# Kernel optimization log

Hardware: AMD Instinct MI355X
Metric: run time of the kernel (lower is better)

## Reference

```python
import jax, jax.numpy as jnp
import numpy as np

B, D, N, H = 2, 512, 2048, 8
DK = D // H
EPS = 1e-5


def conv1x1(x, w, b):
    # kernel-size-1 Conv1d == channel-mixing GEMM: (o,i) x (b,i,n) -> (b,o,n)
    return jnp.einsum('oi,bin->bon', w, x) + b[None, :, None]


def setup_inputs() -> dict:
    key = jax.random.key(0)
    ks = jax.random.split(key, 20)
    s = 0.02
    return {
        'init_query': jax.random.normal(ks[0], (B, D, N), jnp.float32),
        'key_t': jax.random.normal(ks[1], (B, D, N), jnp.float32),
        'value': jax.random.normal(ks[2], (B, D, N), jnp.float32),
        'mask': jax.random.randint(ks[3], (B, 1, N, N), 0, 2, jnp.int32),
        'Wq': jax.random.normal(ks[4], (D, D), jnp.float32) * s,
        'bq': jax.random.normal(ks[5], (D,), jnp.float32) * s,
        'Wk': jax.random.normal(ks[6], (D, D), jnp.float32) * s,
        'bk': jax.random.normal(ks[7], (D,), jnp.float32) * s,
        'Wv': jax.random.normal(ks[8], (D, D), jnp.float32) * s,
        'bv': jax.random.normal(ks[9], (D,), jnp.float32) * s,
        'Wm': jax.random.normal(ks[10], (D, D), jnp.float32) * s,
        'bm': jax.random.normal(ks[11], (D,), jnp.float32) * s,
        'W1': jax.random.normal(ks[12], (2 * D, 2 * D), jnp.float32) * s,
        'b1': jax.random.normal(ks[13], (2 * D,), jnp.float32) * s,
        'gamma': jnp.ones((2 * D,), jnp.float32),
        'beta': jnp.zeros((2 * D,), jnp.float32),
        'rmean': jax.random.normal(ks[14], (2 * D,), jnp.float32) * s,
        'rvar': jnp.abs(jax.random.normal(ks[15], (2 * D,), jnp.float32)) * 0.1 + 0.5,
        'W2': jax.random.normal(ks[16], (D, 2 * D), jnp.float32) * s,
        'b2': jnp.zeros((D,), jnp.float32),  # nn.init.constant_(bias, 0.0)
    }


def reference(init_query, key_t, value, mask, Wq, bq, Wk, bk, Wv, bv, Wm, bm,
              W1, b1, gamma, beta, rmean, rvar, W2, b2):
    # projections, split channels into (d_k, n_heads) exactly like torch .view
    q = conv1x1(init_query, Wq, bq).reshape(B, DK, H, N)
    k = conv1x1(key_t, Wk, bk).reshape(B, DK, H, N)
    v = conv1x1(value, Wv, bv).reshape(B, DK, H, N)
    scores = jnp.einsum('bdhn,bdhm->bhnm', q, k) / jnp.sqrt(jnp.float32(DK))
    scores = jnp.where(mask == 0, jnp.float32(-1e9), scores)
    attn = jax.nn.softmax(scores, axis=-1)
    x = jnp.einsum('bhnm,bdhm->bdhn', attn, v).reshape(B, D, N)
    x = conv1x1(x, Wm, bm)
    x = jnp.concatenate([x, init_query], axis=1)  # (B, 2D, N)
    h = conv1x1(x, W1, b1)
    # BatchNorm1d (inference mode with running stats) + ReLU
    h = (h - rmean[None, :, None]) * (gamma / jnp.sqrt(rvar + EPS))[None, :, None] + beta[None, :, None]
    h = jax.nn.relu(h)
    return conv1x1(h, W2, b2)
```

## Files before the change

### kernel.cpp

```cpp
#include <hip/hip_runtime.h>

typedef unsigned short u16;
typedef unsigned int u32;
typedef unsigned long long u64;
typedef long long i64;
typedef __bf16 bf16x8 __attribute__((ext_vector_type(8)));
typedef u16 u16x8 __attribute__((ext_vector_type(8)));
typedef float f32x4 __attribute__((ext_vector_type(4)));
typedef float f32x16 __attribute__((ext_vector_type(16)));

#define DEV __device__ __forceinline__

constexpr int BB = 2, DD = 512, NN = 2048, HH = 8, DKc = 64, D2 = 1024;

constexpr float QSC = 0.125f * 1.44269504088896340736f;

constexpr i64 MB = 1048576;
constexpr i64 OFF_CAT = 0;
constexpr i64 OFF_XKT = 8 * MB;
constexpr i64 OFF_XVT = 12 * MB;
constexpr i64 OFF_QH  = 16 * MB;
constexpr i64 OFF_KH  = 20 * MB;
constexpr i64 OFF_VT  = 24 * MB;
constexpr i64 OFF_HT  = 28 * MB;
constexpr i64 OFF_OP  = 36 * MB;
constexpr i64 OFF_LP  = 68 * MB;
constexpr i64 OFF_FLG = 68 * MB + 524288;
constexpr i64 OFF_WQP = 69 * MB;
constexpr i64 OFF_WKP = 69 * MB + 524288;
constexpr i64 OFF_WVP = 69 * MB + 1048576;
constexpr i64 OFF_WMT = 69 * MB + 1572864;
constexpr i64 OFF_W1A = 71 * MB;
constexpr i64 OFF_W1C = 72 * MB;
constexpr i64 OFF_W2B = 74 * MB;
constexpr i64 OFF_BQP = 75 * MB;
constexpr i64 OFF_BKP = 75 * MB + 2048;
constexpr i64 OFF_BVP = 75 * MB + 4096;
constexpr i64 OFF_BNA = 75 * MB + 8192;
constexpr i64 OFF_BNC = 75 * MB + 12288;
constexpr i64 OFF_MSK = 76 * MB;

DEV u16 f2bf(float f) {
  u32 u = __float_as_uint(f);
  u = u + 0x7FFFu + ((u >> 16) & 1u);
  return (u16)(u >> 16);
}

DEV float bf2f(u16 u) { return __uint_as_float(((u32)u) << 16); }
DEV float bf2f32(u32 u) { return __uint_as_float(u << 16); }

DEV u32 packbf(float lo, float hi) {
  return __builtin_amdgcn_perm(__float_as_uint(hi), __float_as_uint(lo), 0x07060302u);
}

DEV float fexp2(float x) {
#if __has_builtin(__builtin_amdgcn_exp2f)
  return __builtin_amdgcn_exp2f(x);
#else
  return exp2f(x);
#endif
}

DEV bf16x8 ldfrag(const u16* p) {
  bf16x8 v;
  __builtin_memcpy(&v, __builtin_assume_aligned(p, 16), 16);
  return v;
}

DEV bf16x8 ldfrag2(const u16* p0, const u16* p1) {
  bf16x8 v;
  __builtin_memcpy(&v, __builtin_assume_aligned(p0, 8), 8);
  __builtin_memcpy((char*)&v + 8, __builtin_assume_aligned(p1, 8), 8);
  return v;
}

DEV bf16x8 ones8() {
  u16x8 u = {0x3F80, 0x3F80, 0x3F80, 0x3F80, 0x3F80, 0x3F80, 0x3F80, 0x3F80};
  bf16x8 v;
  __builtin_memcpy(&v, &u, 16);
  return v;
}

DEV void gload16(const void* g, void* lds) {
  __builtin_amdgcn_global_load_lds((__attribute__((address_space(1))) void*)g,
                                   (__attribute__((address_space(3))) void*)lds, 16, 0, 0);
}

DEV f32x4 mfma16(bf16x8 a, bf16x8 b, f32x4 c) {
  return __builtin_amdgcn_mfma_f32_16x16x32_bf16(a, b, c, 0, 0, 0);
}

DEV f32x16 mfma32(bf16x8 a, bf16x8 b, f32x16 c) {
  return __builtin_amdgcn_mfma_f32_32x32x16_bf16(a, b, c, 0, 0, 0);
}

__global__ __launch_bounds__(256) void prep_all(
    const float* __restrict__ Wq, const float* __restrict__ Wk, const float* __restrict__ Wv,
    const float* __restrict__ Wm, const float* __restrict__ W1, const float* __restrict__ W2,
    const float* __restrict__ bq, const float* __restrict__ bk, const float* __restrict__ bv,
    const float* __restrict__ bm, const float* __restrict__ b1, const float* __restrict__ gamma_,
    const float* __restrict__ beta_, const float* __restrict__ rmean,
    const float* __restrict__ rvar, const int* __restrict__ mask,
    const float* __restrict__ iq, const float* __restrict__ kt, const float* __restrict__ vv,
    u16* __restrict__ wqp, u16* __restrict__ wkp, u16* __restrict__ wvp, u16* __restrict__ wmt,
    u16* __restrict__ w1a, u16* __restrict__ w1c, u16* __restrict__ w2b,
    float* __restrict__ bqp, float* __restrict__ bkp, float* __restrict__ bvp,
    float* __restrict__ bna, float* __restrict__ bnc, u32* __restrict__ mw,
    u32* __restrict__ flg,
    u16* __restrict__ cat, u16* __restrict__ xkt, u16* __restrict__ xvt) {
  __shared__ float tile[32][33];
  const int blk = blockIdx.x, t = threadIdx.x;
  if (blk < 768) {
    const int which = blk >> 8, lb = blk & 255;
    const float* W = which == 0 ? Wq : (which == 1 ? Wk : Wv);
    u16* dst = which == 0 ? wqp : (which == 1 ? wkp : wvp);
    for (int e = lb * 256 + t; e < 262144; e += 65536) {
      int op = e >> 9, i = e & 511;
      int dk = op & 63, h = op >> 6;
      dst[e] = f2bf(W[(dk * 8 + h) * 512 + i]);
    }
  } else if (blk < 1024) {
    const int lb = blk - 768;
    for (int e = lb * 256 + t; e < 262144; e += 65536) {
      int cp = e >> 9, o = e & 511;
      int dk = cp & 63, h = cp >> 6;
      wmt[e] = f2bf(Wm[o * 512 + dk * 8 + h]);
    }
  } else if (blk < 1280) {
    const int lb = blk - 1024;
    for (int e = lb * 256 + t; e < 524288; e += 65536) {
      int row = e >> 9, o = e & 511;
      w1a[e] = f2bf(W1[(i64)row * 1024 + o]);
    }
  } else if (blk < 1536) {
    const int lb = blk - 1280;
    for (int e = lb * 256 + t; e < 524288; e += 65536) {
      int row = e >> 9, j = e & 511;
      w1c[(i64)row * 1024 + 512 + j] = f2bf(W1[(i64)row * 1024 + 512 + j]);
    }
  } else if (blk < 1792) {
    const int lb = blk - 1536;
    for (int e = lb * 256 + t; e < 524288; e += 65536) w2b[e] = f2bf(W2[e]);
  } else if (blk < 1808) {
    __shared__ float sm[4][64];
    const int base = (blk - 1792) * 64;
    const int el = t & 63, oq = t >> 6;
    const float* wrow = W1 + (i64)(base + el) * 1024 + oq * 128;
    const float* bmq = bm + oq * 128;
    float s = 0.f;
#pragma unroll 8
    for (int j = 0; j < 128; j += 4) {
      float4 x = *(const float4*)(wrow + j);
      float4 y = *(const float4*)(bmq + j);
      s += x.x * y.x + x.y * y.y + x.z * y.z + x.w * y.w;
    }
    sm[oq][el] = s;
    __syncthreads();
    if (t < 64) {
      int e = base + t;
      float a = gamma_[e] * rsqrtf(rvar[e] + 1e-5f);
      bna[e] = a;
      bnc[e] = (b1[e] - rmean[e]) * a + beta_[e] + a * (sm[0][t] + sm[1][t] + sm[2][t] + sm[3][t]);
    }
  } else if (blk == 1808) {
    for (int e = t; e < 512; e += 256) {
      int src = (e & 63) * 8 + (e >> 6);
      bqp[e] = bq[src]; bkp[e] = bk[src]; bvp[e] = bv[src];
    }
    if (t < 128) flg[t] = 0u;
  } else if (blk < 2833) {
    const int tid = (blk - 1809) * 256 + t;
    const i64 base = (i64)tid * 32;
    const int4* mp = (const int4*)(mask + base);
    u32 word = 0;
#pragma unroll
    for (int j = 0; j < 8; ++j) {
      int4 x = mp[j];
      u32 nib = (x.x != 0 ? 1u : 0u) | (x.y != 0 ? 2u : 0u) | (x.z != 0 ? 4u : 0u) |
                (x.w != 0 ? 8u : 0u);
      word |= nib << (j * 4);
    }
    mw[tid] = word;
  } else {
    const int idx = blk - 2833;
    const int bx = idx & 63, by = (idx >> 6) & 15, bz = idx >> 10;
    const int tensor = bz >> 1, b = bz & 1;
    const float* src = (tensor == 0 ? iq : (tensor == 1 ? kt : vv)) + (i64)b * DD * NN;
    u16* dst; i64 ldd; int coff;
    if (tensor == 0)      { dst = cat + (i64)b * NN * D2; ldd = D2; coff = DD; }
    else if (tensor == 1) { dst = xkt + (i64)b * NN * DD; ldd = DD; coff = 0; }
    else                  { dst = xvt + (i64)b * NN * DD; ldd = DD; coff = 0; }
    const int x0 = bx * 32, y0 = by * 32;
    const int col = t & 31, rg = t >> 5;
#pragma unroll
    for (int i = 0; i < 4; ++i) {
      int row = rg + i * 8;
      tile[row][col] = src[(i64)(y0 + row) * NN + x0 + col];
    }
    __syncthreads();
    const int dp = t & 15, rbase = t >> 4;
    u32* dst32 = (u32*)dst;
    const i64 ldw = ldd >> 1;
    const int cw = (coff + y0) >> 1;
#pragma unroll
    for (int i = 0; i < 2; ++i) {
      int rr = rbase + i * 16;
      dst32[(i64)(x0 + rr) * ldw + cw + dp] = packbf(tile[2 * dp][rr], tile[2 * dp + 1][rr]);
    }
  }
}

template <int AM, int AN>
DEV void gemm_core(const u16* __restrict__ A, i64 lda, const u16* __restrict__ Bp, i64 ldb,
                   int K, u16* As, u16* Bs, f32x4 (&acc)[AM][AN]) {
  constexpr int BM = AM * 32, BN = AN * 32;
  const int t = threadIdx.x, w = t >> 6, l = t & 63, quad = l >> 4, l15 = l & 15;
  const int wm = (w >> 1) * AM * 16, wn = (w & 1) * AN * 16;
  auto stage = [&](int kk, int buf) {
    u16* Ad = As + buf * (BM * 64);
    u16* Bd = Bs + buf * (BN * 64);
#pragma unroll
    for (int j = 0; j < BM / 32; ++j) {
      int ch = j * 256 + w * 64 + l, r = ch >> 3, c = ch & 7;
      gload16(A + (i64)r * lda + kk + ((c ^ (r & 7)) << 3), Ad + (j * 256 + w * 64) * 8);
    }
#pragma unroll
    for (int j = 0; j < BN / 32; ++j) {
      int ch = j * 256 + w * 64 + l, r = ch >> 3, c = ch & 7;
      gload16(Bp + (i64)r * ldb + kk + ((c ^ (r & 7)) << 3), Bd + (j * 256 + w * 64) * 8);
    }
  };
  const int nst = K >> 6;
  stage(0, 0);
  asm volatile("s_waitcnt vmcnt(0)" ::: "memory");
  __builtin_amdgcn_s_barrier();
  for (int s = 0; s < nst; ++s) {
    if (s + 1 < nst) stage((s + 1) << 6, (s + 1) & 1);
    const u16* Ac = As + (s & 1) * (BM * 64);
    const u16* Bc = Bs + (s & 1) * (BN * 64);
#pragma unroll
    for (int kc = 0; kc < 2; ++kc) {
      const int sw = ((kc * 4 + quad) ^ (l15 & 7)) << 3;
      bf16x8 af[AM], bfr[AN];
#pragma unroll
      for (int i = 0; i < AM; ++i) af[i] = ldfrag(&Ac[(wm + i * 16 + l15) * 64 + sw]);
#pragma unroll
      for (int j = 0; j < AN; ++j) bfr[j] = ldfrag(&Bc[(wn + j * 16 + l15) * 64 + sw]);
#pragma unroll
      for (int i = 0; i < AM; ++i)
#pragma unroll
        for (int j = 0; j < AN; ++j) acc[i][j] = mfma16(af[i], bfr[j], acc[i][j]);
    }
    asm volatile("s_waitcnt vmcnt(0) lgkmcnt(0)" ::: "memory");
    __builtin_amdgcn_s_barrier();
  }
}

__global__ __launch_bounds__(256) void qkv_gemm(const u16* __restrict__ cat,
                                                const u16* __restrict__ xkt,
                                                const u16* __restrict__ xvt,
                                                const u16* __restrict__ wqp,
                                                const u16* __restrict__ wkp,
                                                const u16* __restrict__ wvp,
                                                const u16* __restrict__ w1a,
                                                const u16* __restrict__ wmt,
                                                const float* __restrict__ bqp,
                                                const float* __restrict__ bkp,
                                                const float* __restrict__ bvp,
                                                u16* __restrict__ qh, u16* __restrict__ kh,
                                                u16* __restrict__ vt, u16* __restrict__ w1c) {
  __shared__ __align__(16) u16 As[2 * 128 * 64];
  __shared__ __align__(16) u16 Bs[2 * 128 * 64];
  const int flat = blockIdx.x;
  const int t = threadIdx.x, w = t >> 6, l = t & 63, quad = l >> 4, l15 = l & 15;
  const int wm = (w >> 1) * 64, wn = (w & 1) * 64;
  int op, b = 0, mx, ny;
  if (flat < 256) {
    op = flat >> 7;
    b = (flat >> 6) & 1;
    const int r = flat & 63;
    mx = r >> 2; ny = r & 3;
  } else if (flat < 384) {
    op = 2;
    const int r = flat - 256;
    b = r >> 6;
    const int rr = r & 63;
    mx = rr >> 4; ny = rr & 15;
  } else {
    op = 3;
    const int r = flat - 384;
    mx = r >> 2; ny = r & 3;
  }
  const u16 *A, *Bp;
  i64 lda, ldb;
  if (op < 2) {
    A = (op == 0 ? cat + DD : xkt);
    lda = (op == 0 ? D2 : DD);
    A += (i64)b * NN * lda + (i64)mx * 128 * lda;
    Bp = (op == 0 ? wqp : wkp) + (i64)ny * 128 * DD;
    ldb = DD;
  } else if (op == 2) {
    A = wvp + (i64)mx * 128 * DD; lda = DD;
    Bp = xvt + (i64)b * NN * DD + (i64)ny * 128 * DD; ldb = DD;
  } else {
    A = w1a + (i64)mx * 128 * DD; lda = DD;
    Bp = wmt + (i64)ny * 128 * DD; ldb = DD;
  }
  f32x4 acc[4][4] = {};
  gemm_core<4, 4>(A, lda, Bp, ldb, DD, As, Bs, acc);

  const int rowBase = mx * 128 + wm + quad * 4;
  const int colBase = ny * 128 + wn + l15;
  if (op < 2) {
    const float* bias = (op == 0 ? bqp : bkp);
    const float sc = (op == 0 ? QSC : 1.f);
    u16* dst = (op == 0 ? qh : kh) + (i64)b * HH * NN * DKc;
#pragma unroll
    for (int j = 0; j < 4; ++j) {
      const int col = colBase + j * 16;
      const float cA = bias[col];
#pragma unroll
      for (int i = 0; i < 4; ++i)
#pragma unroll
        for (int r = 0; r < 4; ++r) {
          const int row = rowBase + i * 16 + r;
          dst[(i64)(col >> 6) * (NN * 64) + (i64)row * 64 + (col & 63)] =
              f2bf((acc[i][j][r] + cA) * sc);
        }
    }
  } else if (op == 2) {
    u16* dst = vt + (i64)b * HH * DKc * NN;
#pragma unroll
    for (int j = 0; j < 4; ++j) {
      const int col = colBase + j * 16;
#pragma unroll
      for (int i = 0; i < 4; ++i)
#pragma unroll
        for (int r = 0; r < 4; ++r) {
          const int row = rowBase + i * 16 + r;
          dst[(i64)row * NN + col] = f2bf(acc[i][j][r] + bvp[row]);
        }
    }
  } else {
#pragma unroll
    for (int j = 0; j < 4; ++j) {
      const int col = colBase + j * 16;
#pragma unroll
      for (int i = 0; i < 4; ++i)
#pragma unroll
        for (int r = 0; r < 4; ++r) {
          const int row = rowBase + i * 16 + r;
          w1c[(i64)row * D2 + col] = f2bf(acc[i][j][r]);
        }
    }
  }
}

struct GArgs {
  const u16* A; i64 lda, sAb;
  const u16* B; i64 ldb, sBb;
  void* C; i64 ldc, sCb;
  const float* p1; const float* p2;
  int K;
};

template <int MODE, int AM, int AN, int SWZ>
__global__ __launch_bounds__(256) void gemm_bt(GArgs g) {
  __shared__ __align__(16) u16 As[2 * AM * 32 * 64];
  __shared__ __align__(16) u16 Bs[2 * AN * 32 * 64];
  const int t = threadIdx.x, w = t >> 6, l = t & 63, quad = l >> 4, l15 = l & 15;
  const int wm = (w >> 1) * AM * 16, wn = (w & 1) * AN * 16;
  int bx = blockIdx.x, by = blockIdx.y, bz = blockIdx.z;
  if (SWZ == 1) {
    const int i = bx + (by << 3) + (bz << 8);
    const int slot = i & 7, jj = i >> 3;
    by = slot + ((jj & 3) << 3);
    const int j2 = jj >> 2;
    bx = j2 & 7;
    bz = j2 >> 3;
  }
  const u16* A = g.A + (i64)bz * g.sAb + (i64)bx * (AM * 32) * g.lda;
  const u16* Bp = g.B + (i64)bz * g.sBb + (i64)by * (AN * 32) * g.ldb;
  f32x4 acc[AM][AN] = {};
  gemm_core<AM, AN>(A, g.lda, Bp, g.ldb, g.K, As, Bs, acc);

  const int rowBase = bx * (AM * 32) + wm + quad * 4;
  const int colBase = by * (AN * 32) + wn + l15;
#pragma unroll
  for (int j = 0; j < AN; ++j) {
    const int col = colBase + j * 16;
    float cA = 0.f, cB = 0.f;
    if (MODE == 3) { cA = g.p1[col]; cB = g.p2[col]; }
#pragma unroll
    for (int i = 0; i < AM; ++i) {
#pragma unroll
      for (int r = 0; r < 4; ++r) {
        const int row = rowBase + i * 16 + r;
        float v = acc[i][j][r];
        if (MODE == 3) {
          float x = v * cA + cB;
          ((u16*)g.C + (i64)bz * g.sCb)[(i64)row * g.ldc + col] = f2bf(x > 0.f ? x : 0.f);
        } else {
          ((float*)g.C + (i64)bz * g.sCb)[(i64)row * g.ldc + col] = v + g.p1[row];
        }
      }
    }
  }
}

__global__ __launch_bounds__(512) void flash_attn(const u16* __restrict__ Qh,
                                                  const u16* __restrict__ Kh,
                                                  const u16* __restrict__ Vt,
                                                  const u64* __restrict__ MW64,
                                                  u16* __restrict__ Opart,
                                                  float* __restrict__ Lp,
                                                  u32* __restrict__ flags,
                                                  u16* __restrict__ cat) {
  __shared__ __align__(16) u16 smem[4 * 4096];
  u16* Ks0 = smem;
  u16* Ks1 = smem + 4096;
  u16* Vs0 = smem + 8192;
  u16* Vs1 = smem + 12288;
  const int t = threadIdx.x, w = t >> 6, l = t & 63, l31 = l & 31, lh = l >> 5;
  const int flat = blockIdx.x;
  const int h = flat & 7;
  const int j = flat >> 3;
  const int nt = j & 7, zz = j >> 3;
  const int sp = zz & 1, b = zz >> 1;
  const int nl = w * 32 + l31;
  const int n = nt * 256 + nl;
  const u16* Qb = Qh + ((i64)(b * HH + h) * NN + nt * 256 + w * 32) * 64;
  const u16* Kb = Kh + (i64)(b * HH + h) * NN * 64;
  const u16* Vb = Vt + (i64)(b * HH + h) * 64 * NN;
  const u64* mwp = MW64 + (i64)(b * NN + n) * 32;
  const bf16x8 ONE = ones8();
  bf16x8 qf[4];
#pragma unroll
  for (int kc = 0; kc < 4; ++kc)
    __builtin_memcpy(&qf[kc], Qb + (i64)l31 * 64 + kc * 16 + lh * 8, 16);

  f32x16 oacc0 = {}, oacc1 = {}, lacc = {};
  const int mt0 = sp * 16;

  auto stage = [&](u16* Kd, u16* Vd, int mt) {
    const int r = t >> 3, c = t & 7;
    gload16(Kb + (i64)(mt * 64 + r) * 64 + ((c ^ (r & 7)) << 3), Kd + t * 8);
    gload16(Vb + (i64)r * NN + mt * 64 + ((c ^ (r & 7)) << 3), Vd + t * 8);
  };
  auto compute = [&](const u16* Kc, const u16* Vc, int mt) {
    f32x16 s0 = {}, s1 = {};
    __builtin_amdgcn_s_setprio(1);
#pragma unroll
    for (int kc = 0; kc < 4; ++kc) {
      const int sw = l31 & 7;
      bf16x8 k0 = ldfrag(&Kc[l31 * 64 + (((kc * 2 + lh) ^ sw) << 3)]);
      bf16x8 k1 = ldfrag(&Kc[(32 + l31) * 64 + (((kc * 2 + lh) ^ sw) << 3)]);
      s0 = mfma32(k0, qf[kc], s0);
      s1 = mfma32(k1, qf[kc], s1);
    }
    __builtin_amdgcn_s_setprio(0);
    const u64 mrow = mwp[mt];
    u32 pw[16];
#pragma unroll
    for (int k = 0; k < 8; ++k) {
      const int kvb = ((2 * k) & 3) + 8 * ((2 * k) >> 2) + 4 * lh;
      u64 sh = mrow >> kvb;
      u32 mA = (((u32)sh & 1u) | (((u32)sh & 2u) << 15)) * 0xFFFFu;
      u32 shh = (u32)(sh >> 32);
      u32 mB = ((shh & 1u) | ((shh & 2u) << 15)) * 0xFFFFu;
      pw[k] = packbf(fexp2(s0[2 * k]), fexp2(s0[2 * k + 1])) & mA;
      pw[8 + k] = packbf(fexp2(s1[2 * k]), fexp2(s1[2 * k + 1])) & mB;
    }
    bf16x8 pf[4];
#pragma unroll
    for (int c = 0; c < 4; ++c) __builtin_memcpy(&pf[c], &pw[c * 4], 16);
    __builtin_amdgcn_s_setprio(1);
#pragma unroll
    for (int c = 0; c < 4; ++c) lacc = mfma32(ONE, pf[c], lacc);
#pragma unroll
    for (int c = 0; c < 4; ++c) {
      const int sw0 = l31 & 7;
      const u16* r0 = &Vc[l31 * 64];
      const u16* r1 = &Vc[(32 + l31) * 64];
      bf16x8 v0 = ldfrag2(r0 + (((2 * c) ^ sw0) << 3) + lh * 4,
                          r0 + (((2 * c + 1) ^ sw0) << 3) + lh * 4);
      bf16x8 v1 = ldfrag2(r1 + (((2 * c) ^ sw0) << 3) + lh * 4,
                          r1 + (((2 * c + 1) ^ sw0) << 3) + lh * 4);
      oacc0 = mfma32(v0, pf[c], oacc0);
      oacc1 = mfma32(v1, pf[c], oacc1);
    }
    __builtin_amdgcn_s_setprio(0);
  };

  stage(Ks0, Vs0, mt0);
  for (int ii = 0; ii < 8; ++ii) {
    const int m = mt0 + 2 * ii;
    __syncthreads();
    stage(Ks1, Vs1, m + 1);
    compute(Ks0, Vs0, m);
    __syncthreads();
    if (ii < 7) stage(Ks0, Vs0, m + 2);
    compute(Ks1, Vs1, m + 1);
  }

  u16* OpT = Opart + ((i64)((sp * BB + b) * HH + h) * 64) * NN;
#pragma unroll
  for (int r = 0; r < 16; ++r) {
    const int d0 = (r & 3) + 8 * (r >> 2) + 4 * lh;
    OpT[(i64)d0 * NN + n] = f2bf(oacc0[r]);
    OpT[(i64)(d0 + 32) * NN + n] = f2bf(oacc1[r]);
  }
  if (lh == 0) Lp[((i64)(sp * BB + b) * HH + h) * NN + n] = lacc[0];

  __shared__ u32 sflag;
  __syncthreads();
  if (t == 0) {
    __builtin_amdgcn_fence(__ATOMIC_RELEASE, "agent");
    const int pair = ((b * HH + h) << 3) | nt;
    sflag = atomicAdd(&flags[pair], 1u);
  }
  __syncthreads();
  if (sflag == 1u) {
    __builtin_amdgcn_fence(__ATOMIC_ACQUIRE, "agent");
    const int spo = sp ^ 1;
    const u16* OpP = Opart + ((i64)((spo * BB + b) * HH + h) * 64) * NN;
    const float lsum = lacc[0] + Lp[((i64)(spo * BB + b) * HH + h) * NN + n];
    const float rl = __builtin_amdgcn_rcpf(lsum);
    u32* lds32 = (u32*)smem;
#pragma unroll
    for (int e = 0; e < 8; ++e) {
      const int r0 = 2 * e, r1 = 2 * e + 1;
      const int d0 = (r0 & 3) + 8 * (r0 >> 2) + 4 * lh;
      const float a0 = oacc0[r0] + bf2f(OpP[(i64)d0 * NN + n]);
      const float a1 = oacc0[r1] + bf2f(OpP[(i64)(d0 + 1) * NN + n]);
      const float b0 = oacc1[r0] + bf2f(OpP[(i64)(d0 + 32) * NN + n]);
      const float b1 = oacc1[r1] + bf2f(OpP[(i64)(d0 + 33) * NN + n]);
      const int dp0 = d0 >> 1;
      lds32[nl * 32 + (dp0 ^ (nl & 31))] = packbf(a0 * rl, a1 * rl);
      lds32[nl * 32 + ((dp0 + 16) ^ (nl & 31))] = packbf(b0 * rl, b1 * rl);
    }
    __syncthreads();
    u32* catw = (u32*)cat;
#pragma unroll
    for (int i = 0; i < 16; ++i) {
      const int idx = i * 512 + t;
      const int nn = idx >> 5, dp = idx & 31;
      const u32 v = lds32[nn * 32 + (dp ^ (nn & 31))];
      catw[((i64)b * NN + nt * 256 + nn) * (D2 / 2) + h * 32 + dp] = v;
    }
  }
}

extern "C" void kernel_launch(void* const* d_in, const int* in_sizes, int n_in,
                              void* d_out, int out_size, void* d_ws, size_t ws_size,
                              hipStream_t stream) {
  (void)in_sizes; (void)n_in; (void)out_size; (void)ws_size;
  const float* iq    = (const float*)d_in[0];
  const float* kt    = (const float*)d_in[1];
  const float* vv    = (const float*)d_in[2];
  const int*   mask  = (const int*)d_in[3];
  const float* Wq    = (const float*)d_in[4];
  const float* bq    = (const float*)d_in[5];
  const float* Wk    = (const float*)d_in[6];
  const float* bk    = (const float*)d_in[7];
  const float* Wv    = (const float*)d_in[8];
  const float* bv    = (const float*)d_in[9];
  const float* Wm    = (const float*)d_in[10];
  const float* bm    = (const float*)d_in[11];
  const float* W1    = (const float*)d_in[12];
  const float* b1    = (const float*)d_in[13];
  const float* gamma_= (const float*)d_in[14];
  const float* beta_ = (const float*)d_in[15];
  const float* rmean = (const float*)d_in[16];
  const float* rvar  = (const float*)d_in[17];
  const float* W2    = (const float*)d_in[18];
  const float* b2    = (const float*)d_in[19];

  char* ws = (char*)d_ws;
  u16* cat = (u16*)(ws + OFF_CAT);
  u16* xkt = (u16*)(ws + OFF_XKT);
  u16* xvt = (u16*)(ws + OFF_XVT);
  u16* qh  = (u16*)(ws + OFF_QH);
  u16* kh  = (u16*)(ws + OFF_KH);
  u16* vt  = (u16*)(ws + OFF_VT);
  u16* ht  = (u16*)(ws + OFF_HT);
  u16* opart = (u16*)(ws + OFF_OP);
  float* lp  = (float*)(ws + OFF_LP);
  u32* flags = (u32*)(ws + OFF_FLG);
  u16* wqp = (u16*)(ws + OFF_WQP);
  u16* wkp = (u16*)(ws + OFF_WKP);
  u16* wvp = (u16*)(ws + OFF_WVP);
  u16* wmt = (u16*)(ws + OFF_WMT);
  u16* w1a = (u16*)(ws + OFF_W1A);
  u16* w1c = (u16*)(ws + OFF_W1C);
  u16* w2b = (u16*)(ws + OFF_W2B);
  float* bqp = (float*)(ws + OFF_BQP);
  float* bkp = (float*)(ws + OFF_BKP);
  float* bvp = (float*)(ws + OFF_BVP);
  float* bna = (float*)(ws + OFF_BNA);
  float* bnc = (float*)(ws + OFF_BNC);
  u32* mw = (u32*)(ws + OFF_MSK);

  prep_all<<<8977, 256, 0, stream>>>(Wq, Wk, Wv, Wm, W1, W2, bq, bk, bv, bm, b1, gamma_, beta_,
                                     rmean, rvar, mask, iq, kt, vv, wqp, wkp, wvp, wmt, w1a, w1c,
                                     w2b, bqp, bkp, bvp, bna, bnc, mw, flags, cat, xkt, xvt);
  qkv_gemm<<<416, 256, 0, stream>>>(cat, xkt, xvt, wqp, wkp, wvp, w1a, wmt,
                                    bqp, bkp, bvp, qh, kh, vt, w1c);
  flash_attn<<<256, 512, 0, stream>>>(qh, kh, vt, (const u64*)mw, opart, lp, flags, cat);
  GArgs wa{cat, D2, 0, w1c, D2, 0, ht, D2, 0, bna, bnc, D2};
  gemm_bt<3, 4, 2, 0><<<dim3(32, 16, 1), 256, 0, stream>>>(wa);
  GArgs w2a{w2b, D2, 0, ht, D2, (i64)NN * D2, d_out, NN, (i64)DD * NN, b2, nullptr, D2};
  gemm_bt<4, 2, 2, 1><<<dim3(8, 32, 2), 256, 0, stream>>>(w2a);
}
```

Measured before the change: 226.2 us.

## Split KV range within a block instead of across blocks with global merge

Previously each attention block handled 256 queries over half the keys and the two split blocks merged partial outputs through global memory, an atomic flag and fences. Now each block handles 128 queries over all keys, and its two wave halves each process alternate key sub-tiles, then merge partial sums through shared memory. This removes the global partial-output writes and reads, the atomic handshake and the flag initialisation. In exchange, shared memory use doubles to 64KB, each block runs twice as many KV iterations, and the in-block reduction adds barriers.

```diff
diff --git a/kernel.cpp b/kernel.cpp
--- a/kernel.cpp
+++ b/kernel.cpp
@@ -23,9 +23,6 @@
 constexpr i64 OFF_KH  = 20 * MB;
 constexpr i64 OFF_VT  = 24 * MB;
 constexpr i64 OFF_HT  = 28 * MB;
-constexpr i64 OFF_OP  = 36 * MB;
-constexpr i64 OFF_LP  = 68 * MB;
-constexpr i64 OFF_FLG = 68 * MB + 524288;
 constexpr i64 OFF_WQP = 69 * MB;
 constexpr i64 OFF_WKP = 69 * MB + 524288;
 constexpr i64 OFF_WVP = 69 * MB + 1048576;
@@ -106,7 +103,6 @@
     u16* __restrict__ w1a, u16* __restrict__ w1c, u16* __restrict__ w2b,
     float* __restrict__ bqp, float* __restrict__ bkp, float* __restrict__ bvp,
     float* __restrict__ bna, float* __restrict__ bnc, u32* __restrict__ mw,
-    u32* __restrict__ flg,
     u16* __restrict__ cat, u16* __restrict__ xkt, u16* __restrict__ xvt) {
   __shared__ float tile[32][33];
   const int blk = blockIdx.x, t = threadIdx.x;
@@ -167,7 +163,6 @@
       int src = (e & 63) * 8 + (e >> 6);
       bqp[e] = bq[src]; bkp[e] = bk[src]; bvp[e] = bv[src];
     }
-    if (t < 128) flg[t] = 0u;
   } else if (blk < 2833) {
     const int tid = (blk - 1809) * 256 + t;
     const i64 base = (i64)tid * 32;
@@ -412,24 +407,19 @@
                                                   const u16* __restrict__ Kh,
                                                   const u16* __restrict__ Vt,
                                                   const u64* __restrict__ MW64,
-                                                  u16* __restrict__ Opart,
-                                                  float* __restrict__ Lp,
-                                                  u32* __restrict__ flags,
                                                   u16* __restrict__ cat) {
-  __shared__ __align__(16) u16 smem[4 * 4096];
-  u16* Ks0 = smem;
-  u16* Ks1 = smem + 4096;
-  u16* Vs0 = smem + 8192;
-  u16* Vs1 = smem + 12288;
+  __shared__ __align__(16) u16 smem[4 * 8192];
+  u16* S0 = smem;
+  u16* S1 = smem + 16384;
   const int t = threadIdx.x, w = t >> 6, l = t & 63, l31 = l & 31, lh = l >> 5;
   const int flat = blockIdx.x;
   const int h = flat & 7;
   const int j = flat >> 3;
-  const int nt = j & 7, zz = j >> 3;
-  const int sp = zz & 1, b = zz >> 1;
-  const int nl = w * 32 + l31;
-  const int n = nt * 256 + nl;
-  const u16* Qb = Qh + ((i64)(b * HH + h) * NN + nt * 256 + w * 32) * 64;
+  const int nt = j & 15, b = j >> 4;
+  const int g = w & 3, half = w >> 2;
+  const int nl = g * 32 + l31;
+  const int n = nt * 128 + nl;
+  const u16* Qb = Qh + ((i64)(b * HH + h) * NN + nt * 128 + g * 32) * 64;
   const u16* Kb = Kh + (i64)(b * HH + h) * NN * 64;
   const u16* Vb = Vt + (i64)(b * HH + h) * 64 * NN;
   const u64* mwp = MW64 + (i64)(b * NN + n) * 32;
@@ -440,114 +430,107 @@
     __builtin_memcpy(&qf[kc], Qb + (i64)l31 * 64 + kc * 16 + lh * 8, 16);
 
   f32x16 oacc0 = {}, oacc1 = {}, lacc = {};
-  const int mt0 = sp * 16;
+  const int hrow = half * 32 + l31;
+  const int sw = l31 & 7;
 
   auto stage = [&](u16* Kd, u16* Vd, int mt) {
     const int r = t >> 3, c = t & 7;
     gload16(Kb + (i64)(mt * 64 + r) * 64 + ((c ^ (r & 7)) << 3), Kd + t * 8);
     gload16(Vb + (i64)r * NN + mt * 64 + ((c ^ (r & 7)) << 3), Vd + t * 8);
   };
-  auto compute = [&](const u16* Kc, const u16* Vc, int mt) {
-    f32x16 s0 = {}, s1 = {};
+  auto stage_pair = [&](u16* S, int mt) {
+    stage(S, S + 4096, mt);
+    stage(S + 8192, S + 12288, mt + 1);
+  };
+  auto compute_half = [&](const u16* Kc, const u16* Vc, int mt) {
+    f32x16 s = {};
     __builtin_amdgcn_s_setprio(1);
 #pragma unroll
     for (int kc = 0; kc < 4; ++kc) {
-      const int sw = l31 & 7;
-      bf16x8 k0 = ldfrag(&Kc[l31 * 64 + (((kc * 2 + lh) ^ sw) << 3)]);
-      bf16x8 k1 = ldfrag(&Kc[(32 + l31) * 64 + (((kc * 2 + lh) ^ sw) << 3)]);
-      s0 = mfma32(k0, qf[kc], s0);
-      s1 = mfma32(k1, qf[kc], s1);
+      bf16x8 k0 = ldfrag(&Kc[hrow * 64 + (((kc * 2 + lh) ^ sw) << 3)]);
+      s = mfma32(k0, qf[kc], s);
     }
     __builtin_amdgcn_s_setprio(0);
     const u64 mrow = mwp[mt];
-    u32 pw[16];
+    u32 pw[8];
 #pragma unroll
     for (int k = 0; k < 8; ++k) {
       const int kvb = ((2 * k) & 3) + 8 * ((2 * k) >> 2) + 4 * lh;
-      u64 sh = mrow >> kvb;
-      u32 mA = (((u32)sh & 1u) | (((u32)sh & 2u) << 15)) * 0xFFFFu;
-      u32 shh = (u32)(sh >> 32);
-      u32 mB = ((shh & 1u) | ((shh & 2u) << 15)) * 0xFFFFu;
-      pw[k] = packbf(fexp2(s0[2 * k]), fexp2(s0[2 * k + 1])) & mA;
-      pw[8 + k] = packbf(fexp2(s1[2 * k]), fexp2(s1[2 * k + 1])) & mB;
-    }
-    bf16x8 pf[4];
-#pragma unroll
-    for (int c = 0; c < 4; ++c) __builtin_memcpy(&pf[c], &pw[c * 4], 16);
+      const u32 m2 = (u32)(mrow >> (kvb + half * 32));
+      const u32 mA = ((m2 & 1u) | ((m2 & 2u) << 15)) * 0xFFFFu;
+      pw[k] = packbf(fexp2(s[2 * k]), fexp2(s[2 * k + 1])) & mA;
+    }
+    bf16x8 pf[2];
+#pragma unroll
+    for (int c = 0; c < 2; ++c) __builtin_memcpy(&pf[c], &pw[c * 4], 16);
     __builtin_amdgcn_s_setprio(1);
-#pragma unroll
-    for (int c = 0; c < 4; ++c) lacc = mfma32(ONE, pf[c], lacc);
-#pragma unroll
-    for (int c = 0; c < 4; ++c) {
-      const int sw0 = l31 & 7;
+    lacc = mfma32(ONE, pf[0], lacc);
+    lacc = mfma32(ONE, pf[1], lacc);
+#pragma unroll
+    for (int cc = 0; cc < 2; ++cc) {
+      const int ch0 = 2 * (2 * half + cc), ch1 = ch0 + 1;
       const u16* r0 = &Vc[l31 * 64];
       const u16* r1 = &Vc[(32 + l31) * 64];
-      bf16x8 v0 = ldfrag2(r0 + (((2 * c) ^ sw0) << 3) + lh * 4,
-                          r0 + (((2 * c + 1) ^ sw0) << 3) + lh * 4);
-      bf16x8 v1 = ldfrag2(r1 + (((2 * c) ^ sw0) << 3) + lh * 4,
-                          r1 + (((2 * c + 1) ^ sw0) << 3) + lh * 4);
-      oacc0 = mfma32(v0, pf[c], oacc0);
-      oacc1 = mfma32(v1, pf[c], oacc1);
+      bf16x8 v0 = ldfrag2(r0 + ((ch0 ^ sw) << 3) + lh * 4, r0 + ((ch1 ^ sw) << 3) + lh * 4);
+      bf16x8 v1 = ldfrag2(r1 + ((ch0 ^ sw) << 3) + lh * 4, r1 + ((ch1 ^ sw) << 3) + lh * 4);
+      oacc0 = mfma32(v0, pf[cc], oacc0);
+      oacc1 = mfma32(v1, pf[cc], oacc1);
     }
     __builtin_amdgcn_s_setprio(0);
   };
-
-  stage(Ks0, Vs0, mt0);
+  auto compute_pair = [&](const u16* S, int mt) {
+    compute_half(S, S + 4096, mt);
+    compute_half(S + 8192, S + 12288, mt + 1);
+  };
+
+  stage_pair(S0, 0);
   for (int ii = 0; ii < 8; ++ii) {
-    const int m = mt0 + 2 * ii;
+    const int m = 4 * ii;
     __syncthreads();
-    stage(Ks1, Vs1, m + 1);
-    compute(Ks0, Vs0, m);
+    stage_pair(S1, m + 2);
+    compute_pair(S0, m);
     __syncthreads();
-    if (ii < 7) stage(Ks0, Vs0, m + 2);
-    compute(Ks1, Vs1, m + 1);
-  }
-
-  u16* OpT = Opart + ((i64)((sp * BB + b) * HH + h) * 64) * NN;
-#pragma unroll
-  for (int r = 0; r < 16; ++r) {
-    const int d0 = (r & 3) + 8 * (r >> 2) + 4 * lh;
-    OpT[(i64)d0 * NN + n] = f2bf(oacc0[r]);
-    OpT[(i64)(d0 + 32) * NN + n] = f2bf(oacc1[r]);
-  }
-  if (lh == 0) Lp[((i64)(sp * BB + b) * HH + h) * NN + n] = lacc[0];
-
-  __shared__ u32 sflag;
+    if (ii < 7) stage_pair(S0, m + 4);
+    compute_pair(S1, m + 2);
+  }
+
   __syncthreads();
-  if (t == 0) {
-    __builtin_amdgcn_fence(__ATOMIC_RELEASE, "agent");
-    const int pair = ((b * HH + h) << 3) | nt;
-    sflag = atomicAdd(&flags[pair], 1u);
+  u32* ex = (u32*)smem;
+  float* exl = (float*)((char*)smem + 16384);
+  if (half == 1) {
+#pragma unroll
+    for (int e = 0; e < 8; ++e) {
+      const int r0 = 2 * e, r1 = r0 + 1;
+      const int dp = ((r0 & 3) + 8 * (r0 >> 2) + 4 * lh) >> 1;
+      ex[nl * 32 + (dp ^ (nl & 31))] = packbf(oacc0[r0], oacc0[r1]);
+      ex[nl * 32 + ((dp + 16) ^ (nl & 31))] = packbf(oacc1[r0], oacc1[r1]);
+    }
+    if (lh == 0) exl[nl] = lacc[0];
   }
   __syncthreads();
-  if (sflag == 1u) {
-    __builtin_amdgcn_fence(__ATOMIC_ACQUIRE, "agent");
-    const int spo = sp ^ 1;
-    const u16* OpP = Opart + ((i64)((spo * BB + b) * HH + h) * 64) * NN;
-    const float lsum = lacc[0] + Lp[((i64)(spo * BB + b) * HH + h) * NN + n];
+  u32* lt = (u32*)((char*)smem + 32768);
+  if (half == 0) {
+    const float lsum = lacc[0] + exl[nl];
     const float rl = __builtin_amdgcn_rcpf(lsum);
-    u32* lds32 = (u32*)smem;
 #pragma unroll
     for (int e = 0; e < 8; ++e) {
-      const int r0 = 2 * e, r1 = 2 * e + 1;
-      const int d0 = (r0 & 3) + 8 * (r0 >> 2) + 4 * lh;
-      const float a0 = oacc0[r0] + bf2f(OpP[(i64)d0 * NN + n]);
-      const float a1 = oacc0[r1] + bf2f(OpP[(i64)(d0 + 1) * NN + n]);
-      const float b0 = oacc1[r0] + bf2f(OpP[(i64)(d0 + 32) * NN + n]);
-      const float b1 = oacc1[r1] + bf2f(OpP[(i64)(d0 + 33) * NN + n]);
-      const int dp0 = d0 >> 1;
-      lds32[nl * 32 + (dp0 ^ (nl & 31))] = packbf(a0 * rl, a1 * rl);
-      lds32[nl * 32 + ((dp0 + 16) ^ (nl & 31))] = packbf(b0 * rl, b1 * rl);
-    }
-    __syncthreads();
-    u32* catw = (u32*)cat;
-#pragma unroll
-    for (int i = 0; i < 16; ++i) {
-      const int idx = i * 512 + t;
-      const int nn = idx >> 5, dp = idx & 31;
-      const u32 v = lds32[nn * 32 + (dp ^ (nn & 31))];
-      catw[((i64)b * NN + nt * 256 + nn) * (D2 / 2) + h * 32 + dp] = v;
-    }
+      const int r0 = 2 * e, r1 = r0 + 1;
+      const int dp = ((r0 & 3) + 8 * (r0 >> 2) + 4 * lh) >> 1;
+      const u32 va = ex[nl * 32 + (dp ^ (nl & 31))];
+      const u32 vb = ex[nl * 32 + ((dp + 16) ^ (nl & 31))];
+      lt[nl * 32 + (dp ^ (nl & 31))] =
+          packbf((oacc0[r0] + bf2f32(va & 0xFFFFu)) * rl, (oacc0[r1] + bf2f32(va >> 16)) * rl);
+      lt[nl * 32 + ((dp + 16) ^ (nl & 31))] =
+          packbf((oacc1[r0] + bf2f32(vb & 0xFFFFu)) * rl, (oacc1[r1] + bf2f32(vb >> 16)) * rl);
+    }
+  }
+  __syncthreads();
+  u32* catw = (u32*)cat;
+#pragma unroll
+  for (int i = 0; i < 8; ++i) {
+    const int idx = i * 512 + t;
+    const int nn = idx >> 5, dp = idx & 31;
+    catw[((i64)b * NN + nt * 128 + nn) * (D2 / 2) + h * 32 + dp] = lt[nn * 32 + (dp ^ (nn & 31))];
   }
 }
 
@@ -584,9 +567,6 @@
   u16* kh  = (u16*)(ws + OFF_KH);
   u16* vt  = (u16*)(ws + OFF_VT);
   u16* ht  = (u16*)(ws + OFF_HT);
-  u16* opart = (u16*)(ws + OFF_OP);
-  float* lp  = (float*)(ws + OFF_LP);
-  u32* flags = (u32*)(ws + OFF_FLG);
   u16* wqp = (u16*)(ws + OFF_WQP);
   u16* wkp = (u16*)(ws + OFF_WKP);
   u16* wvp = (u16*)(ws + OFF_WVP);
@@ -603,10 +583,10 @@
 
   prep_all<<<8977, 256, 0, stream>>>(Wq, Wk, Wv, Wm, W1, W2, bq, bk, bv, bm, b1, gamma_, beta_,
                                      rmean, rvar, mask, iq, kt, vv, wqp, wkp, wvp, wmt, w1a, w1c,
-                                     w2b, bqp, bkp, bvp, bna, bnc, mw, flags, cat, xkt, xvt);
+                                     w2b, bqp, bkp, bvp, bna, bnc, mw, cat, xkt, xvt);
   qkv_gemm<<<416, 256, 0, stream>>>(cat, xkt, xvt, wqp, wkp, wvp, w1a, wmt,
                                     bqp, bkp, bvp, qh, kh, vt, w1c);
-  flash_attn<<<256, 512, 0, stream>>>(qh, kh, vt, (const u64*)mw, opart, lp, flags, cat);
+  flash_attn<<<256, 512, 0, stream>>>(qh, kh, vt, (const u64*)mw, cat);
   GArgs wa{cat, D2, 0, w1c, D2, 0, ht, D2, 0, bna, bnc, D2};
   gemm_bt<3, 4, 2, 0><<<dim3(32, 16, 1), 256, 0, stream>>>(wa);
   GArgs w2a{w2b, D2, 0, ht, D2, (i64)NN * D2, d_out, NN, (i64)DD * NN, b2, nullptr, D2};
```

Result: faster. 210.3 us (median of 2 runs) (-7.0%).
